# Kernel tuning notes

Hardware: AMD Instinct MI355X
Metric: run time of the kernel (lower is better)

## Reference

```python
import jax, jax.numpy as jnp
import numpy as np

B, N, D = 4, 4096, 512
K = 16384          # codebook size
NUM_Q = 2          # residual quantizers (shared codebook)


def setup_inputs() -> dict:
    key = jax.random.key(0)
    ks = jax.random.split(key, 6)
    s = 1.0 / np.sqrt(D)
    return {
        "x": jax.random.normal(ks[0], (B, N, D), dtype=jnp.float32),
        "enc_w": jax.random.normal(ks[1], (D, D), dtype=jnp.float32) * s,
        "enc_b": jnp.zeros((D,), dtype=jnp.float32),
        "codebook": jax.random.normal(ks[2], (K, D), dtype=jnp.float32),
        "dec_w": jax.random.normal(ks[3], (D, D), dtype=jnp.float32) * s,
        "dec_b": jnp.zeros((D,), dtype=jnp.float32),
    }


def _residual_vq(z, codebook):
    # z: [B, N, D] -> flatten tokens
    flat = z.reshape(-1, z.shape[-1])          # [T, D]
    c_sq = jnp.sum(codebook * codebook, axis=-1)  # [K]
    q_sum = jnp.zeros_like(flat)
    residual = flat
    for _ in range(NUM_Q):
        # argmin of ||r - c||^2 == argmin of (||c||^2 - 2 r.c); skip ||r||^2
        dists = c_sq[None, :] - 2.0 * (residual @ codebook.T)  # [T, K]
        idx = jnp.argmin(dists, axis=-1)                       # [T]
        q = codebook[idx]                                      # gather [T, D]
        q_sum = q_sum + q
        residual = residual - q
    return q_sum.reshape(z.shape)


def reference(x, enc_w, enc_b, codebook, dec_w, dec_b):
    z = x @ enc_w.T + enc_b                     # encoder Linear(512 -> 512)
    q = _residual_vq(z, codebook)               # sum of per-stage code vectors
    z_tilde = z + jax.lax.stop_gradient(q - z)  # straight-through estimator
    x_recon = z_tilde @ dec_w.T + dec_b         # decoder Linear(512 -> 512)
    return x_recon
```

## Files before the change

kernel.cpp:

```cpp
#include <hip/hip_runtime.h>
#include <stdint.h>

constexpr int TT = 16384;
constexpr int DD = 512;
constexpr int KK = 16384;
constexpr int TOPK = 8;

typedef __bf16 bf16x8 __attribute__((ext_vector_type(8)));
typedef __bf16 bf16x4 __attribute__((ext_vector_type(4)));
typedef float f32x4 __attribute__((ext_vector_type(4)));

typedef const __attribute__((address_space(1))) void* gas_ptr;
typedef __attribute__((address_space(3))) void* las_ptr;

__device__ __forceinline__ unsigned long long pack_di(float d, int idx) {
    uint32_t u = __float_as_uint(d);
    u = (u & 0x80000000u) ? ~u : (u | 0x80000000u);
    return ((unsigned long long)u << 32) | (uint32_t)idx;
}

__device__ __forceinline__ unsigned long long umin64(unsigned long long a,
                                                     unsigned long long b) {
    return a < b ? a : b;
}
__device__ __forceinline__ uint32_t umin32(uint32_t a, uint32_t b) { return a < b ? a : b; }
__device__ __forceinline__ uint32_t umax32(uint32_t a, uint32_t b) { return a > b ? a : b; }

__device__ __forceinline__ uint32_t sortable(float d) {
    uint32_t u = __float_as_uint(d);
    return u ^ ((uint32_t)((int32_t)u >> 31) | 0x80000000u);
}

template<int MODE>
__global__ __launch_bounds__(256)
void gemm_mfma(const float* __restrict__ A, const float* __restrict__ A2,
               const float* __restrict__ W, const float* __restrict__ bias,
               float* __restrict__ out0, float* __restrict__ out1,
               __bf16* __restrict__ out2)
{
    __shared__ __bf16 Ah[128 * 64], Al[128 * 64];
    __shared__ __bf16 Bh[128 * 64], Bl[128 * 64];
    const int tid = threadIdx.x;
    const int lane = tid & 63;
    const int w = tid >> 6;
    const int row0 = blockIdx.y * 128;
    const int col0 = blockIdx.x * 128;

    f32x4 acc[2][8] = {};

    const int sr = tid >> 4;
    const int scol = (tid & 15) * 4;
    const int lcol = (((scol >> 3) ^ (sr & 7)) << 3) + (scol & 7);

    int a_off[2], b_off[8];
    #pragma unroll
    for (int mi = 0; mi < 2; ++mi) {
        const int ar = w * 32 + mi * 16 + (lane & 15);
        a_off[mi] = ar * 64 + (((lane >> 4) ^ (ar & 7)) << 3);
    }
    #pragma unroll
    for (int ni = 0; ni < 8; ++ni) {
        const int br = ni * 16 + (lane & 15);
        b_off[ni] = br * 64 + (((lane >> 4) ^ (br & 7)) << 3);
    }

    for (int kb = 0; kb < 512; kb += 64) {
        __syncthreads();
        #pragma unroll
        for (int i = 0; i < 8; ++i) {
            const int r = i * 16 + sr;
            float4 v = *(const float4*)(A + (size_t)(row0 + r) * 512 + kb + scol);
            if (MODE == 1) {
                const float4 u = *(const float4*)(A2 + (size_t)(row0 + r) * 512 + kb + scol);
                v.x -= u.x; v.y -= u.y; v.z -= u.z; v.w -= u.w;
            }
            bf16x4 hv, lv;
            hv[0] = (__bf16)v.x; hv[1] = (__bf16)v.y; hv[2] = (__bf16)v.z; hv[3] = (__bf16)v.w;
            lv[0] = (__bf16)(v.x - (float)hv[0]); lv[1] = (__bf16)(v.y - (float)hv[1]);
            lv[2] = (__bf16)(v.z - (float)hv[2]); lv[3] = (__bf16)(v.w - (float)hv[3]);
            *(bf16x4*)(Ah + r * 64 + lcol) = hv;
            *(bf16x4*)(Al + r * 64 + lcol) = lv;

            const float4 x = *(const float4*)(W + (size_t)(col0 + r) * 512 + kb + scol);
            bf16x4 hw, lw;
            hw[0] = (__bf16)x.x; hw[1] = (__bf16)x.y; hw[2] = (__bf16)x.z; hw[3] = (__bf16)x.w;
            lw[0] = (__bf16)(x.x - (float)hw[0]); lw[1] = (__bf16)(x.y - (float)hw[1]);
            lw[2] = (__bf16)(x.z - (float)hw[2]); lw[3] = (__bf16)(x.w - (float)hw[3]);
            *(bf16x4*)(Bh + r * 64 + lcol) = hw;
            *(bf16x4*)(Bl + r * 64 + lcol) = lw;
        }
        __syncthreads();
        #pragma unroll
        for (int s = 0; s < 2; ++s) {
            const int sx = s * 32;
            bf16x8 ah[2], al[2];
            #pragma unroll
            for (int mi = 0; mi < 2; ++mi) {
                ah[mi] = *(const bf16x8*)(Ah + (a_off[mi] ^ sx));
                al[mi] = *(const bf16x8*)(Al + (a_off[mi] ^ sx));
            }
            #pragma unroll
            for (int ni = 0; ni < 8; ++ni) {
                const bf16x8 bh = *(const bf16x8*)(Bh + (b_off[ni] ^ sx));
                const bf16x8 bl = *(const bf16x8*)(Bl + (b_off[ni] ^ sx));
                #pragma unroll
                for (int mi = 0; mi < 2; ++mi) {
                    acc[mi][ni] = __builtin_amdgcn_mfma_f32_16x16x32_bf16(ah[mi], bh, acc[mi][ni], 0, 0, 0);
                    acc[mi][ni] = __builtin_amdgcn_mfma_f32_16x16x32_bf16(ah[mi], bl, acc[mi][ni], 0, 0, 0);
                    acc[mi][ni] = __builtin_amdgcn_mfma_f32_16x16x32_bf16(al[mi], bh, acc[mi][ni], 0, 0, 0);
                }
            }
        }
    }

    #pragma unroll
    for (int mi = 0; mi < 2; ++mi) {
        #pragma unroll
        for (int reg = 0; reg < 4; ++reg) {
            const int row = row0 + w * 32 + mi * 16 + (lane >> 4) * 4 + reg;
            #pragma unroll
            for (int ni = 0; ni < 8; ++ni) {
                const int col = col0 + ni * 16 + (lane & 15);
                const float o = acc[mi][ni][reg] + bias[col];
                out0[(size_t)row * 512 + col] = o;
                if (MODE == 0) {
                    out1[(size_t)row * 512 + col] = o;
                    out2[(size_t)row * 512 + col] = (__bf16)o;
                }
            }
        }
    }
}

constexpr int CHAIN = 4;
constexpr size_t TILE_A = 256 * 512;

__global__ __launch_bounds__(512, 2)
void dist_approx8(const __bf16* __restrict__ Rh,
                  const __bf16* __restrict__ Ch,
                  const float* __restrict__ csq,
                  uint32_t* __restrict__ winners)
{
    __shared__ __bf16 As[2][256 * 64];
    __shared__ __bf16 Bs[2][256 * 64];

    const int tid  = threadIdx.x;
    const int lane = tid & 63;
    const int w    = tid >> 6;
    const int wm   = w >> 2;
    const int wn   = w & 3;

    const int b    = blockIdx.x;
    const int xcd  = b & 7;
    const int i    = b >> 3;
    const int ct   = xcd * 8 + (i & 7);
    const int tg   = i >> 3;
    const int col0 = ct << 8;
    const int rowb = tg << 10;

    f32x4 acc[8][4] = {};

    const int s_r = tid >> 3;
    const int s_c = (tid & 7) ^ (s_r & 7);
    const __bf16* aS = Rh + (size_t)(rowb + s_r) * 512 + s_c * 8;
    const __bf16* bS = Ch + (size_t)(col0 + s_r) * 512 + s_c * 8;
    __bf16* const lA0 = &As[0][0]; __bf16* const lA1 = &As[1][0];
    __bf16* const lB0 = &Bs[0][0]; __bf16* const lB1 = &Bs[1][0];

#define AOFF(q) ((size_t)((q) >> 3) * TILE_A + (size_t)((q) & 7) * 64)

#define STAGE(SRC, UOFF, DST)                                                      \
    {                                                                              \
        __builtin_amdgcn_global_load_lds((gas_ptr)((SRC) + (UOFF)),                \
                                         (las_ptr)((DST) + w * 8 * 64), 16, 0, 0); \
        __builtin_amdgcn_global_load_lds((gas_ptr)((SRC) + (UOFF) + 64 * 512),     \
                                         (las_ptr)((DST) + (64 + w * 8) * 64), 16, 0, 0); \
    }

    int aoff[8], boff[4];
    #pragma unroll
    for (int mi = 0; mi < 8; ++mi) {
        const int r = wm * 128 + mi * 16 + (lane & 15);
        aoff[mi] = r * 64 + (((lane >> 4) ^ (r & 7)) << 3);
    }
    #pragma unroll
    for (int ni = 0; ni < 4; ++ni) {
        const int r = wn * 64 + ni * 16 + (lane & 15);
        boff[ni] = r * 64 + (((lane >> 4) ^ (r & 7)) << 3);
    }

#define BAR __builtin_amdgcn_s_barrier()
#define LGKM0 { asm volatile("s_waitcnt lgkmcnt(0)" ::: "memory"); \
                __builtin_amdgcn_sched_barrier(0); }
#define MFMA_QUAD(AF, A0, BV)                                                  \
    {                                                                          \
        __builtin_amdgcn_s_setprio(1);                                         \
        _Pragma("unroll")                                                      \
        for (int mi = 0; mi < 4; ++mi) {                                       \
            _Pragma("unroll")                                                  \
            for (int ni = 0; ni < 4; ++ni)                                     \
                acc[(A0) + mi][ni] = __builtin_amdgcn_mfma_f32_16x16x32_bf16(  \
                    (AF)[(A0) + mi], (BV)[ni], acc[(A0) + mi][ni], 0, 0, 0);   \
        }                                                                      \
        __builtin_amdgcn_s_setprio(0);                                         \
    }

    float csv[4];
    #pragma unroll
    for (int ni = 0; ni < 4; ++ni)
        csv[ni] = csq[col0 + wn * 64 + ni * 16 + (lane & 15)];
    const int gt = (col0 >> 6) + wn;

    STAGE(aS, AOFF(0),             lA0);
    STAGE(aS, AOFF(0) + 128 * 512, lA0 + 128 * 64);
    STAGE(bS, 0,                   lB0);
    STAGE(bS, 128 * 512,           lB0 + 128 * 64);
    STAGE(aS, AOFF(1),             lA1);
    STAGE(aS, AOFF(1) + 128 * 512, lA1 + 128 * 64);
    asm volatile("s_waitcnt vmcnt(4)" ::: "memory");
    BAR;

    bf16x8 a0[8], a1[8], b0[4], b1[4];

    for (int it = 0; it < 4 * CHAIN; ++it) {
        const bool more = it < 4 * CHAIN - 1;
        const size_t oB1 = (size_t)((2 * it + 1) & 7) * 64;
        const size_t oA2 = AOFF(2 * it + 2);
        const size_t oB2 = (size_t)((2 * it + 2) & 7) * 64;
        const size_t oA3 = AOFF(2 * it + 3);

        #pragma unroll
        for (int mi = 0; mi < 8; ++mi) a0[mi] = *(const bf16x8*)(lA0 + aoff[mi]);
        #pragma unroll
        for (int ni = 0; ni < 4; ++ni) b0[ni] = *(const bf16x8*)(lB0 + boff[ni]);
        STAGE(bS, oB1, lB1);
        BAR; LGKM0;
        MFMA_QUAD(a0, 0, b0);
        BAR;

        #pragma unroll
        for (int mi = 0; mi < 8; ++mi) a1[mi] = *(const bf16x8*)(lA0 + (aoff[mi] ^ 32));
        STAGE(bS, 128 * 512 + oB1, lB1 + 128 * 64);
        BAR; LGKM0;
        MFMA_QUAD(a0, 4, b0);
        BAR;

        #pragma unroll
        for (int ni = 0; ni < 4; ++ni) b1[ni] = *(const bf16x8*)(lB0 + (boff[ni] ^ 32));
        if (more) STAGE(aS, oA2, lA0);
        BAR; LGKM0;
        MFMA_QUAD(a1, 0, b1);
        BAR;

        if (more) STAGE(aS, oA2 + 128 * 512, lA0 + 128 * 64);
        BAR;
        MFMA_QUAD(a1, 4, b1);
        if (more) { asm volatile("s_waitcnt vmcnt(4)" ::: "memory"); }
        else      { asm volatile("s_waitcnt vmcnt(0)" ::: "memory"); }
        BAR;

        #pragma unroll
        for (int mi = 0; mi < 8; ++mi) a0[mi] = *(const bf16x8*)(lA1 + aoff[mi]);
        #pragma unroll
        for (int ni = 0; ni < 4; ++ni) b0[ni] = *(const bf16x8*)(lB1 + boff[ni]);
        if (more) STAGE(bS, oB2, lB0);
        BAR; LGKM0;
        MFMA_QUAD(a0, 0, b0);
        BAR;

        #pragma unroll
        for (int mi = 0; mi < 8; ++mi) a1[mi] = *(const bf16x8*)(lA1 + (aoff[mi] ^ 32));
        if (more) STAGE(bS, 128 * 512 + oB2, lB0 + 128 * 64);
        BAR; LGKM0;
        MFMA_QUAD(a0, 4, b0);
        BAR;

        #pragma unroll
        for (int ni = 0; ni < 4; ++ni) b1[ni] = *(const bf16x8*)(lB1 + (boff[ni] ^ 32));
        if (more) STAGE(aS, oA3, lA1);
        BAR; LGKM0;
        MFMA_QUAD(a1, 0, b1);
        BAR;

        if (more) STAGE(aS, oA3 + 128 * 512, lA1 + 128 * 64);
        BAR;
        MFMA_QUAD(a1, 4, b1);
        if (more) { asm volatile("s_waitcnt vmcnt(4)" ::: "memory"); }
        BAR;

        if ((it & 3) == 3) {
            const int r0t = rowb + (it >> 2) * 256;
            #pragma unroll
            for (int mi = 0; mi < 8; ++mi) {
                #pragma unroll
                for (int reg = 0; reg < 4; ++reg) {
                    uint32_t bk = 0xFFFFFFFFu, sk = 0xFFFFFFFFu;
                    #pragma unroll
                    for (int ni = 0; ni < 4; ++ni) {
                        const float d = fmaf(-2.0f, acc[mi][ni][reg], csv[ni]);
                        const uint32_t key = (sortable(d) & 0xFFFFFFC0u)
                                           | (uint32_t)(ni * 16 + (lane & 15));
                        const uint32_t nb = umin32(bk, key);
                        sk = umin32(sk, umax32(bk, key));
                        bk = nb;
                    }
                    #pragma unroll
                    for (int m = 1; m < 16; m <<= 1) {
                        const uint32_t ob = __shfl_xor((int)bk, m, 16);
                        const uint32_t os = __shfl_xor((int)sk, m, 16);
                        const uint32_t nb = umin32(bk, ob);
                        sk = umin32(umin32(sk, os), umax32(bk, ob));
                        bk = nb;
                    }
                    if ((lane & 15) == 0) {
                        const int row = r0t + wm * 128 + mi * 16 + (lane >> 4) * 4 + reg;
                        uint2 v; v.x = bk; v.y = sk;
                        *(uint2*)(winners + (size_t)row * 512 + gt * 2) = v;
                    }
                }
            }
            #pragma unroll
            for (int mi = 0; mi < 8; ++mi)
                #pragma unroll
                for (int ni = 0; ni < 4; ++ni)
                    acc[mi][ni] = (f32x4){0.f, 0.f, 0.f, 0.f};
        }
    }
#undef STAGE
#undef AOFF
#undef BAR
#undef LGKM0
#undef MFMA_QUAD
}

__global__ __launch_bounds__(256)
void select_rescore(const uint32_t* __restrict__ winners,
                    const float* __restrict__ CB, const float* __restrict__ csq,
                    float* __restrict__ R, __bf16* __restrict__ R16)
{
    const int w = threadIdx.x >> 6;
    const int lane = threadIdx.x & 63;
    const int token = blockIdx.x * 4 + w;

    const uint32_t* wt = winners + (size_t)token * 512;
    uint4 q0 = *(const uint4*)(wt + lane * 8);
    uint4 q1 = *(const uint4*)(wt + lane * 8 + 4);
    uint32_t k32[8] = {q0.x, q0.y, q0.z, q0.w, q1.x, q1.y, q1.z, q1.w};

    unsigned long long v[8];
    #pragma unroll
    for (int j = 0; j < 8; ++j) {
        const int gcol = ((lane * 8 + j) >> 1) * 64 + (int)(k32[j] & 63u);
        v[j] = ((unsigned long long)k32[j] << 32) | (uint32_t)gcol;
    }

    unsigned long long cand[TOPK];
    #pragma unroll
    for (int t = 0; t < TOPK; ++t) {
        unsigned long long mm = v[0];
        #pragma unroll
        for (int j = 1; j < 8; ++j) mm = umin64(mm, v[j]);
        #pragma unroll
        for (int m = 1; m < 64; m <<= 1)
            mm = umin64(mm, __shfl_xor(mm, m, 64));
        cand[t] = mm;
        #pragma unroll
        for (int j = 0; j < 8; ++j) if (v[j] == mm) v[j] = ~0ull;
    }

    float4 r0 = *(const float4*)(R + (size_t)token * 512 + lane * 8);
    float4 r1 = *(const float4*)(R + (size_t)token * 512 + lane * 8 + 4);

    unsigned long long best = ~0ull;
    #pragma unroll
    for (int t = 0; t < TOPK; ++t) {
        const int col = (int)(cand[t] & 0xFFFFFFFFull);
        const float4 c0 = *(const float4*)(CB + (size_t)col * 512 + lane * 8);
        const float4 c1 = *(const float4*)(CB + (size_t)col * 512 + lane * 8 + 4);
        float dot = r0.x * c0.x;
        dot = fmaf(r0.y, c0.y, dot); dot = fmaf(r0.z, c0.z, dot);
        dot = fmaf(r0.w, c0.w, dot); dot = fmaf(r1.x, c1.x, dot);
        dot = fmaf(r1.y, c1.y, dot); dot = fmaf(r1.z, c1.z, dot);
        dot = fmaf(r1.w, c1.w, dot);
        #pragma unroll
        for (int m = 1; m < 64; m <<= 1) dot += __shfl_xor(dot, m, 64);
        const float d = fmaf(-2.0f, dot, csq[col]);
        best = umin64(best, pack_di(d, col));
    }

    const int bcol = (int)(best & 0xFFFFFFFFull);
    const float4 c0 = *(const float4*)(CB + (size_t)bcol * 512 + lane * 8);
    const float4 c1 = *(const float4*)(CB + (size_t)bcol * 512 + lane * 8 + 4);
    r0.x -= c0.x; r0.y -= c0.y; r0.z -= c0.z; r0.w -= c0.w;
    r1.x -= c1.x; r1.y -= c1.y; r1.z -= c1.z; r1.w -= c1.w;
    *(float4*)(R + (size_t)token * 512 + lane * 8) = r0;
    *(float4*)(R + (size_t)token * 512 + lane * 8 + 4) = r1;
    bf16x8 h;
    h[0] = (__bf16)r0.x; h[1] = (__bf16)r0.y; h[2] = (__bf16)r0.z; h[3] = (__bf16)r0.w;
    h[4] = (__bf16)r1.x; h[5] = (__bf16)r1.y; h[6] = (__bf16)r1.z; h[7] = (__bf16)r1.w;
    *(bf16x8*)(R16 + (size_t)token * 512 + lane * 8) = h;
}

__global__ __launch_bounds__(256)
void prep_cb(const float* __restrict__ CB, float* __restrict__ c_sq,
             __bf16* __restrict__ cb16)
{
    const int wave = threadIdx.x >> 6;
    const int lane = threadIdx.x & 63;
    const int row = blockIdx.x * 4 + wave;
    const float* p = CB + (size_t)row * DD + lane * 8;
    const float4 a = *(const float4*)p;
    const float4 b = *(const float4*)(p + 4);
    bf16x8 h;
    h[0] = (__bf16)a.x; h[1] = (__bf16)a.y; h[2] = (__bf16)a.z; h[3] = (__bf16)a.w;
    h[4] = (__bf16)b.x; h[5] = (__bf16)b.y; h[6] = (__bf16)b.z; h[7] = (__bf16)b.w;
    *(bf16x8*)(cb16 + (size_t)row * DD + lane * 8) = h;
    float s = a.x*a.x + a.y*a.y + a.z*a.z + a.w*a.w
            + b.x*b.x + b.y*b.y + b.z*b.z + b.w*b.w;
    #pragma unroll
    for (int m = 1; m < 64; m <<= 1) s += __shfl_xor(s, m, 64);
    if (lane == 0) c_sq[row] = s;
}

extern "C" void kernel_launch(void* const* d_in, const int* in_sizes, int n_in,
                              void* d_out, int out_size, void* d_ws, size_t ws_size,
                              hipStream_t stream)
{
    const float* x    = (const float*)d_in[0];
    const float* encw = (const float*)d_in[1];
    const float* encb = (const float*)d_in[2];
    const float* cb   = (const float*)d_in[3];
    const float* decw = (const float*)d_in[4];
    const float* decb = (const float*)d_in[5];
    float* out = (float*)d_out;

    float* z    = (float*)d_ws;
    float* r    = z + (size_t)TT * DD;
    __bf16* cb16 = (__bf16*)(r + (size_t)TT * DD);
    __bf16* r16  = cb16 + (size_t)KK * DD;
    float* csq  = (float*)(r16 + (size_t)TT * DD);
    uint32_t* winners = (uint32_t*)d_out;

    const dim3 blk(256);

    gemm_mfma<0><<<dim3(DD / 128, TT / 128), blk, 0, stream>>>(
        x, nullptr, encw, encb, z, r, r16);

    prep_cb<<<dim3(KK / 4), blk, 0, stream>>>(cb, csq, cb16);

    for (int s = 0; s < 2; ++s) {
        dist_approx8<<<dim3((KK / 256) * (TT / 256 / CHAIN)), dim3(512), 0, stream>>>(
            r16, cb16, csq, winners);
        select_rescore<<<dim3(TT / 4), blk, 0, stream>>>(winners, cb, csq, r, r16);
    }

    gemm_mfma<1><<<dim3(DD / 128, TT / 128), blk, 0, stream>>>(
        z, r, decw, decb, out, nullptr, nullptr);
}
```

Baseline: 1.047 ms.

## Double per-block row chain and coarsen barrier schedule in distance kernel

Each block now covers 2048 token rows instead of 1024 (CHAIN 4→8), so every codebook tile loaded into LDS is reused across more rows. The main loop is restructured from fine-grained barrier phases into two half-steps per buffer: stage the global loads early, load the A/B fragments, run two MFMA quads, then a single barrier before refilling the other buffer. The aim is to cut barrier count and stalls between LDS reads and MFMAs. The grid shrinks by half, which could leave CUs underfilled, and the looser ordering relies on the vmcnt waits still guarding the buffer reuse.

Result: faster. 1.007 ms (-3.8%).

```diff
diff --git a/kernel.cpp b/kernel.cpp
--- a/kernel.cpp
+++ b/kernel.cpp
@@ -132,7 +132,7 @@
     }
 }
 
-constexpr int CHAIN = 4;
+constexpr int CHAIN = 8;
 constexpr size_t TILE_A = 256 * 512;
 
 __global__ __launch_bounds__(512, 2)
@@ -156,7 +156,7 @@
     const int ct   = xcd * 8 + (i & 7);
     const int tg   = i >> 3;
     const int col0 = ct << 8;
-    const int rowb = tg << 10;
+    const int rowb = tg << 11;
 
     f32x4 acc[8][4] = {};
 
@@ -229,61 +229,55 @@
         const size_t oB2 = (size_t)((2 * it + 2) & 7) * 64;
         const size_t oA3 = AOFF(2 * it + 3);
 
+        STAGE(bS, oB1,             lB1);
+        STAGE(bS, 128 * 512 + oB1, lB1 + 128 * 64);
         #pragma unroll
         for (int mi = 0; mi < 8; ++mi) a0[mi] = *(const bf16x8*)(lA0 + aoff[mi]);
         #pragma unroll
         for (int ni = 0; ni < 4; ++ni) b0[ni] = *(const bf16x8*)(lB0 + boff[ni]);
-        STAGE(bS, oB1, lB1);
-        BAR; LGKM0;
+        LGKM0;
         MFMA_QUAD(a0, 0, b0);
+        MFMA_QUAD(a0, 4, b0);
+
+        #pragma unroll
+        for (int mi = 0; mi < 8; ++mi) a1[mi] = *(const bf16x8*)(lA0 + (aoff[mi] ^ 32));
+        #pragma unroll
+        for (int ni = 0; ni < 4; ++ni) b1[ni] = *(const bf16x8*)(lB0 + (boff[ni] ^ 32));
+        LGKM0;
         BAR;
-
-        #pragma unroll
-        for (int mi = 0; mi < 8; ++mi) a1[mi] = *(const bf16x8*)(lA0 + (aoff[mi] ^ 32));
-        STAGE(bS, 128 * 512 + oB1, lB1 + 128 * 64);
-        BAR; LGKM0;
-        MFMA_QUAD(a0, 4, b0);
-        BAR;
-
-        #pragma unroll
-        for (int ni = 0; ni < 4; ++ni) b1[ni] = *(const bf16x8*)(lB0 + (boff[ni] ^ 32));
-        if (more) STAGE(aS, oA2, lA0);
-        BAR; LGKM0;
+        if (more) {
+            STAGE(aS, oA2,             lA0);
+            STAGE(aS, oA2 + 128 * 512, lA0 + 128 * 64);
+        }
         MFMA_QUAD(a1, 0, b1);
-        BAR;
-
-        if (more) STAGE(aS, oA2 + 128 * 512, lA0 + 128 * 64);
-        BAR;
         MFMA_QUAD(a1, 4, b1);
         if (more) { asm volatile("s_waitcnt vmcnt(4)" ::: "memory"); }
         else      { asm volatile("s_waitcnt vmcnt(0)" ::: "memory"); }
         BAR;
 
+        if (more) {
+            STAGE(bS, oB2,             lB0);
+            STAGE(bS, 128 * 512 + oB2, lB0 + 128 * 64);
+        }
         #pragma unroll
         for (int mi = 0; mi < 8; ++mi) a0[mi] = *(const bf16x8*)(lA1 + aoff[mi]);
         #pragma unroll
         for (int ni = 0; ni < 4; ++ni) b0[ni] = *(const bf16x8*)(lB1 + boff[ni]);
-        if (more) STAGE(bS, oB2, lB0);
-        BAR; LGKM0;
+        LGKM0;
         MFMA_QUAD(a0, 0, b0);
+        MFMA_QUAD(a0, 4, b0);
+
+        #pragma unroll
+        for (int mi = 0; mi < 8; ++mi) a1[mi] = *(const bf16x8*)(lA1 + (aoff[mi] ^ 32));
+        #pragma unroll
+        for (int ni = 0; ni < 4; ++ni) b1[ni] = *(const bf16x8*)(lB1 + (boff[ni] ^ 32));
+        LGKM0;
         BAR;
-
-        #pragma unroll
-        for (int mi = 0; mi < 8; ++mi) a1[mi] = *(const bf16x8*)(lA1 + (aoff[mi] ^ 32));
-        if (more) STAGE(bS, 128 * 512 + oB2, lB0 + 128 * 64);
-        BAR; LGKM0;
-        MFMA_QUAD(a0, 4, b0);
-        BAR;
-
-        #pragma unroll
-        for (int ni = 0; ni < 4; ++ni) b1[ni] = *(const bf16x8*)(lB1 + (boff[ni] ^ 32));
-        if (more) STAGE(aS, oA3, lA1);
-        BAR; LGKM0;
+        if (more) {
+            STAGE(aS, oA3,             lA1);
+            STAGE(aS, oA3 + 128 * 512, lA1 + 128 * 64);
+        }
         MFMA_QUAD(a1, 0, b1);
-        BAR;
-
-        if (more) STAGE(aS, oA3 + 128 * 512, lA1 + 128 * 64);
-        BAR;
         MFMA_QUAD(a1, 4, b1);
         if (more) { asm volatile("s_waitcnt vmcnt(4)" ::: "memory"); }
         BAR;
```
